# Kernel tuning notes

Measured on AMD Instinct MI355X. Metric: run time of the kernel, lower is better.

The kernel has to match this reference:

```python
import jax, jax.numpy as jnp
import numpy as np


def setup_inputs() -> dict:
    key = jax.random.key(0)
    kx, kq, kv = jax.random.split(key, 3)
    B, S, D = 4, 2048, 64
    # positive inputs + nonnegative W_Q guarantee diagonal scores > threshold t=1,
    # so no softmax column is fully -inf (the original would NaN on symmetric data).
    x = jax.random.uniform(kx, (B, S, D), dtype=jnp.float32)
    std = 1.0 / np.sqrt(S)  # xavier_normal for an SxS matrix: sqrt(2/(S+S))
    W_Q = jnp.abs(jax.random.normal(kq, (S, S), dtype=jnp.float32) * std)
    W_V = jax.random.normal(kv, (S, S), dtype=jnp.float32) * std
    return {"x": x, "W_Q": W_Q, "W_V": W_V}


def reference(x, W_Q, W_V):
    B, S, D = x.shape
    t = 1.0  # sigma threshold
    neg_inf = jnp.asarray(-jnp.inf, x.dtype)

    # V = W_V @ T  (contract over the token axis)
    V = jnp.einsum('st,btd->bsd', W_V, x)

    # G = running mean of tokens (cumsum / position). Original divides by
    # arange(0, S) which is a divide-by-zero bug at position 0; we use the
    # intended running-mean denominator 1..S.
    denom = jnp.arange(1, S + 1, dtype=x.dtype)[None, :, None]  # [1,S,1]
    G = jnp.cumsum(x, axis=1) / denom

    Q = jnp.einsum('st,btd->bsd', W_Q, G)          # [B,S,D]
    scores = jnp.einsum('bid,bjd->bij', Q, x)      # Q @ K^T, K = x

    # sigma: values <= t -> -inf
    scores = jnp.where(scores <= t, neg_inf, scores)

    # causal mask M: -inf strictly above the diagonal
    causal = jnp.triu(jnp.full((S, S), neg_inf, dtype=x.dtype), k=1)
    A = scores + causal

    # NOTE: original softmax is over dim=1 (the query axis), kept faithfully.
    P = jax.nn.softmax(A / jnp.sqrt(jnp.asarray(S, x.dtype)), axis=1)
    return jnp.einsum('bij,bjd->bid', P, V)
```

## Files before the change

kernel.cpp:

```cpp
#include <hip/hip_runtime.h>

typedef unsigned short u16;
typedef __bf16 bf16;
typedef bf16 bf16x8 __attribute__((ext_vector_type(8)));
typedef float f32x4 __attribute__((ext_vector_type(4)));

#define S 2048
#define D 64
#define BATCH 4
#define SCL 0.022097086912079612f

__device__ __forceinline__ u16 f2bf(float f) {
  union { float f; unsigned u; } v; v.f = f;
  return (u16)((v.u + 0x7FFFu + ((v.u >> 16) & 1u)) >> 16);
}

__device__ __forceinline__ void gld16(const u16* g, u16* l) {
  __builtin_amdgcn_global_load_lds(
      (const __attribute__((address_space(1))) unsigned int*)(const void*)g,
      (__attribute__((address_space(3))) unsigned int*)(void*)l, 16, 0, 0);
}

__global__ void k_pre(const float* __restrict__ x,
                      const float* __restrict__ wq, const float* __restrict__ wv,
                      u16* __restrict__ wqp, u16* __restrict__ wvb,
                      u16* __restrict__ xb, u16* __restrict__ xTb,
                      float* __restrict__ out) {
  int bx = blockIdx.x, t = threadIdx.x;
  if (bx < 512) {
    int m = bx * 4 + (t >> 6);
    int l = t & 63;
    const float* row = wq + (size_t)m * S;
    u16* orow = wqp + (size_t)m * S;
    float carry = 0.f;
    for (int c = 31; c >= 0; --c) {
      int tt = c * 64 + l;
      float a = row[tt] / (float)(tt + 1);
      float s = a;
#pragma unroll
      for (int off = 1; off < 64; off <<= 1) {
        float o = __shfl_down(s, off);
        s += (l + off < 64) ? o : 0.f;
      }
      float tot = __shfl(s, 0);
      orow[tt] = f2bf(s + carry);
      carry += tot;
    }
  } else if (bx < 2560) {
    size_t idx = ((size_t)(bx - 512) * 256 + t) * 8;
    const float* src = wv + idx;
    float4 a = *(const float4*)src;
    float4 b = *(const float4*)(src + 4);
    union { u16 s[8]; uint4 v; } u;
    u.s[0]=f2bf(a.x); u.s[1]=f2bf(a.y); u.s[2]=f2bf(a.z); u.s[3]=f2bf(a.w);
    u.s[4]=f2bf(b.x); u.s[5]=f2bf(b.y); u.s[6]=f2bf(b.z); u.s[7]=f2bf(b.w);
    *(uint4*)(wvb + idx) = u.v;
  } else if (bx < 2688) {
    int job = (bx - 2560) * 4 + (t >> 6);
    int chunk = job >> 2, b = job & 3, d = t & 63;
    const float* xp = x + ((size_t)b * S + (size_t)chunk * 16) * D + d;
#pragma unroll
    for (int s = 0; s < 16; ++s) {
      float v = xp[(size_t)s * D];
      int sg = chunk * 16 + s;
      u16 h = f2bf(v);
      xb[((size_t)b * S + sg) * D + d] = h;
      xTb[((size_t)b * D + d) * S + sg] = h;
    }
  } else {
    size_t i = (((size_t)(bx - 2688) * 256) + t) * 4;
    *(float4*)(out + i) = make_float4(0.f, 0.f, 0.f, 0.f);
  }
}

__global__ __launch_bounds__(128) void k_wg(
    const u16* __restrict__ wqp, const u16* __restrict__ wvb,
    const u16* __restrict__ xTb,
    u16* __restrict__ Qb, u16* __restrict__ VTb) {
  __shared__ u16 Ab[2][64 * 64];
  __shared__ u16 Bb[2][32 * 64];
  int bx = blockIdx.x;
  int nt = bx >> 6, mm = bx & 63, mt = mm >> 1, mat = mm & 1;
  int t = threadIdx.x;
  int w = t >> 6, l = t & 63;
  int lr = l & 15, lg = l >> 4;
  const u16* A = (mat ? wvb : wqp) + (size_t)(mt * 64) * S;
  const u16* BT = xTb + (size_t)(nt * 32) * S;
  int rA = t >> 3;
  int sb = t & 7;
  int swz = (sb ^ (rA & 7)) * 8;
  const u16* Ag = A + (size_t)rA * S + swz;
  const u16* Bg = BT + (size_t)rA * S + swz;
  f32x4 acc[2][2] = {};

  auto stage = [&](int buf, int kt) {
#pragma unroll
    for (int i = 0; i < 4; ++i)
      gld16(Ag + kt * 64 + (size_t)i * 16 * S, &Ab[buf][i * 1024 + t * 8]);
#pragma unroll
    for (int i = 0; i < 2; ++i)
      gld16(Bg + kt * 64 + (size_t)i * 16 * S, &Bb[buf][i * 1024 + t * 8]);
  };

  stage(0, 0);
  __syncthreads();
  int buf = 0;
  for (int kt = 0; kt < 32; ++kt) {
    if (kt < 31) stage(buf ^ 1, kt + 1);
    bf16x8 af[2][2], bfv[2][2];
#pragma unroll
    for (int mf = 0; mf < 2; ++mf)
#pragma unroll
      for (int ks = 0; ks < 2; ++ks) {
        int row = w * 32 + mf * 16 + lr;
        af[mf][ks] = *(const bf16x8*)&Ab[buf][row * 64 + (((ks * 4 + lg) ^ (lr & 7)) * 8)];
      }
#pragma unroll
    for (int nf = 0; nf < 2; ++nf)
#pragma unroll
      for (int ks = 0; ks < 2; ++ks) {
        int row = nf * 16 + lr;
        bfv[nf][ks] = *(const bf16x8*)&Bb[buf][row * 64 + (((ks * 4 + lg) ^ (lr & 7)) * 8)];
      }
#pragma unroll
    for (int ks = 0; ks < 2; ++ks)
#pragma unroll
      for (int mf = 0; mf < 2; ++mf)
#pragma unroll
        for (int nf = 0; nf < 2; ++nf)
          acc[mf][nf] = __builtin_amdgcn_mfma_f32_16x16x32_bf16(af[mf][ks], bfv[nf][ks], acc[mf][nf], 0, 0, 0);
    __syncthreads();
    buf ^= 1;
  }
#pragma unroll
  for (int mf = 0; mf < 2; ++mf) {
    int mbase = mt * 64 + w * 32 + mf * 16 + lg * 4;
#pragma unroll
    for (int nf = 0; nf < 2; ++nf) {
      int n = nt * 32 + nf * 16 + lr;
      int b = n >> 6, d = n & 63;
      if (mat == 0) {
#pragma unroll
        for (int r = 0; r < 4; ++r)
          Qb[((size_t)b * S + mbase + r) * D + d] = f2bf(acc[mf][nf][r]);
      } else {
        union { u16 s[4]; ushort4 v; } u;
#pragma unroll
        for (int r = 0; r < 4; ++r) u.s[r] = f2bf(acc[mf][nf][r]);
        *(ushort4*)&VTb[((size_t)b * D + d) * S + mbase] = u.v;
      }
    }
  }
}

__global__ __launch_bounds__(256) void k_stats(
    const u16* __restrict__ xb, const u16* __restrict__ Qb,
    float* __restrict__ rzbuf) {
  __shared__ float zs[4][16];
  int jg = blockIdx.x, b = blockIdx.y;
  int tid = threadIdx.x;
  int w = tid >> 6, l = tid & 63;
  int lr = l & 15, lg = l >> 4;
  int j0 = jg * 16;
  const u16* xbase = xb + (size_t)b * S * D;
  const u16* qbase = Qb + (size_t)b * S * D;
  bf16x8 xa0 = *(const bf16x8*)(xbase + (size_t)(j0 + lr) * D + lg * 8);
  bf16x8 xa1 = *(const bf16x8*)(xbase + (size_t)(j0 + lr) * D + 32 + lg * 8);
  float z[4] = {0.f, 0.f, 0.f, 0.f};
  for (int i16 = j0 + w * 16; i16 < S; i16 += 64) {
    bf16x8 q0 = *(const bf16x8*)(qbase + (size_t)(i16 + lr) * D + lg * 8);
    bf16x8 q1 = *(const bf16x8*)(qbase + (size_t)(i16 + lr) * D + 32 + lg * 8);
    f32x4 c = {};
    c = __builtin_amdgcn_mfma_f32_16x16x32_bf16(xa0, q0, c, 0, 0, 0);
    c = __builtin_amdgcn_mfma_f32_16x16x32_bf16(xa1, q1, c, 0, 0, 0);
    int i = i16 + lr;
#pragma unroll
    for (int r = 0; r < 4; ++r) {
      int j = j0 + lg * 4 + r;
      float sc = c[r];
      z[r] += (i >= j && sc > 1.0f) ? __expf(sc * SCL) : 0.f;
    }
  }
#pragma unroll
  for (int r = 0; r < 4; ++r) {
    z[r] += __shfl_xor(z[r], 1);
    z[r] += __shfl_xor(z[r], 2);
    z[r] += __shfl_xor(z[r], 4);
    z[r] += __shfl_xor(z[r], 8);
  }
  if (lr == 0) {
#pragma unroll
    for (int r = 0; r < 4; ++r) zs[w][lg * 4 + r] = z[r];
  }
  __syncthreads();
  if (tid < 16) {
    float zf = zs[0][tid] + zs[1][tid] + zs[2][tid] + zs[3][tid];
    rzbuf[(size_t)b * S + j0 + tid] = 1.0f / zf;
  }
}

__global__ __launch_bounds__(256) void k_out(
    const u16* __restrict__ xb, const u16* __restrict__ Qb, const u16* __restrict__ VTb,
    const float* __restrict__ rzbuf, float* __restrict__ out) {
  __shared__ u16 Plds[4][16][72];
  int bx = 143 - blockIdx.x, b = blockIdx.y;
  int it = 0, jc = 0, base = 0;
  for (int tt = 0; tt < 32; ++tt) {
    int nc = (tt + 4) >> 2;
    if (bx < base + nc) { it = tt; jc = bx - base; break; }
    base += nc;
  }
  int w = threadIdx.x >> 6, l = threadIdx.x & 63;
  int lr = l & 15, lg = l >> 4;
  int i0 = it * 64 + w * 16;
  const u16* xbase = xb + (size_t)b * S * D;
  const u16* qbase = Qb + (size_t)b * S * D;
  const u16* vbase = VTb + (size_t)b * D * S;
  const float* rzb = rzbuf + (size_t)b * S;
  bf16x8 qa0 = *(const bf16x8*)(qbase + (size_t)(i0 + lr) * D + lg * 8);
  bf16x8 qa1 = *(const bf16x8*)(qbase + (size_t)(i0 + lr) * D + 32 + lg * 8);
  f32x4 acc[4] = {};
  int jt_end = min(jc * 4 + 4, it + 1);
  for (int jt = jc * 4; jt < jt_end; ++jt) {
#pragma unroll
    for (int js = 0; js < 4; ++js) {
      int j16 = jt * 64 + js * 16;
      bf16x8 xb0 = *(const bf16x8*)(xbase + (size_t)(j16 + lr) * D + lg * 8);
      bf16x8 xb1 = *(const bf16x8*)(xbase + (size_t)(j16 + lr) * D + 32 + lg * 8);
      f32x4 c = {};
      c = __builtin_amdgcn_mfma_f32_16x16x32_bf16(qa0, xb0, c, 0, 0, 0);
      c = __builtin_amdgcn_mfma_f32_16x16x32_bf16(qa1, xb1, c, 0, 0, 0);
      int j = j16 + lr;
      float rzj = rzb[j];
#pragma unroll
      for (int r = 0; r < 4; ++r) {
        int i = i0 + lg * 4 + r;
        float sc = c[r];
        float wgt = (j <= i && sc > 1.0f) ? __expf(sc * SCL) * rzj : 0.f;
        Plds[w][lg * 4 + r][js * 16 + lr] = f2bf(wgt);
      }
    }
    asm volatile("s_waitcnt lgkmcnt(0)" ::: "memory");
#pragma unroll
    for (int kk = 0; kk < 2; ++kk) {
      bf16x8 pa = *(const bf16x8*)(&Plds[w][lr][kk * 32 + lg * 8]);
#pragma unroll
      for (int dt = 0; dt < 4; ++dt) {
        bf16x8 vbf = *(const bf16x8*)(vbase + (size_t)(dt * 16 + lr) * S + jt * 64 + kk * 32 + lg * 8);
        acc[dt] = __builtin_amdgcn_mfma_f32_16x16x32_bf16(pa, vbf, acc[dt], 0, 0, 0);
      }
    }
    asm volatile("s_waitcnt lgkmcnt(0)" ::: "memory");
  }
  float* obase = out + (size_t)b * S * D;
#pragma unroll
  for (int dt = 0; dt < 4; ++dt)
#pragma unroll
    for (int r = 0; r < 4; ++r) {
      int i = i0 + lg * 4 + r;
      atomicAdd(&obase[(size_t)i * D + dt * 16 + lr], acc[dt][r]);
    }
}

extern "C" void kernel_launch(void* const* d_in, const int* in_sizes, int n_in,
                              void* d_out, int out_size, void* d_ws, size_t ws_size,
                              hipStream_t stream) {
  const float* x  = (const float*)d_in[0];
  const float* wq = (const float*)d_in[1];
  const float* wv = (const float*)d_in[2];
  float* out = (float*)d_out;
  char* ws = (char*)d_ws;
  size_t off = 0;
  auto alloc = [&](size_t bytes) -> void* {
    void* p = ws + off; off += (bytes + 255) & ~255ULL; return p;
  };
  u16* xb   = (u16*)alloc((size_t)BATCH * S * D * 2);
  u16* xTb  = (u16*)alloc((size_t)BATCH * S * D * 2);
  u16* Qb   = (u16*)alloc((size_t)BATCH * S * D * 2);
  u16* VTb  = (u16*)alloc((size_t)BATCH * S * D * 2);
  float* rzbuf = (float*)alloc((size_t)BATCH * S * 4);
  u16* wqp  = (u16*)alloc((size_t)S * S * 2);
  u16* wvb  = (u16*)alloc((size_t)S * S * 2);

  k_pre<<<3200, 256, 0, stream>>>(x, wq, wv, wqp, wvb, xb, xTb, out);
  k_wg<<<512, 128, 0, stream>>>(wqp, wvb, xTb, Qb, VTb);
  k_stats<<<dim3(128, BATCH), 256, 0, stream>>>(xb, Qb, rzbuf);
  k_out<<<dim3(144, BATCH), 256, 0, stream>>>(xb, Qb, VTb, rzbuf, out);
}
```

Baseline: 81.90 us.

## Fuse stats and output kernels with per-tile counters; vectorize W_Q suffix scan

Merges the column-normalizer kernel and the output kernel into one launch. Stats blocks publish 1/Z per 64-column tile by bumping an atomic counter. Output blocks compute their QK^T tiles first, then spin-wait on that counter before applying the normalizer, which removes a launch boundary and lets the two phases overlap. The W_Q prefix-scan preprocessing is also changed to load float4 per lane and run 8 wave scans instead of 32. The spin-wait risks stalls or deadlock if output blocks occupy the GPU before the stats blocks are scheduled; the fixed block ordering is meant to mitigate this.

```diff
diff --git a/kernel.cpp b/kernel.cpp
--- a/kernel.cpp
+++ b/kernel.cpp
@@ -25,25 +25,42 @@
                       const float* __restrict__ wq, const float* __restrict__ wv,
                       u16* __restrict__ wqp, u16* __restrict__ wvb,
                       u16* __restrict__ xb, u16* __restrict__ xTb,
-                      float* __restrict__ out) {
+                      float* __restrict__ out, int* __restrict__ cnt) {
   int bx = blockIdx.x, t = threadIdx.x;
   if (bx < 512) {
     int m = bx * 4 + (t >> 6);
     int l = t & 63;
     const float* row = wq + (size_t)m * S;
     u16* orow = wqp + (size_t)m * S;
+    float4 f[8];
+#pragma unroll
+    for (int c = 0; c < 8; ++c) f[c] = *(const float4*)(row + c * 256 + l * 4);
+#pragma unroll
+    for (int c = 0; c < 8; ++c) {
+      int base = c * 256 + l * 4;
+      f[c].x /= (float)(base + 1); f[c].y /= (float)(base + 2);
+      f[c].z /= (float)(base + 3); f[c].w /= (float)(base + 4);
+    }
     float carry = 0.f;
-    for (int c = 31; c >= 0; --c) {
-      int tt = c * 64 + l;
-      float a = row[tt] / (float)(tt + 1);
-      float s = a;
+#pragma unroll
+    for (int c = 7; c >= 0; --c) {
+      float4 v = f[c];
+      float sl = v.x + v.y + v.z + v.w;
+      float s = sl;
 #pragma unroll
       for (int off = 1; off < 64; off <<= 1) {
         float o = __shfl_down(s, off);
         s += (l + off < 64) ? o : 0.f;
       }
       float tot = __shfl(s, 0);
-      orow[tt] = f2bf(s + carry);
+      float excl = s - sl;
+      float s3 = v.w, s2 = v.z + s3, s1 = v.y + s2, s0 = v.x + s1;
+      union { u16 q[4]; ushort4 u4; } o;
+      o.q[0] = f2bf(carry + excl + s0);
+      o.q[1] = f2bf(carry + excl + s1);
+      o.q[2] = f2bf(carry + excl + s2);
+      o.q[3] = f2bf(carry + excl + s3);
+      *(ushort4*)(orow + c * 256 + l * 4) = o.u4;
       carry += tot;
     }
   } else if (bx < 2560) {
@@ -68,6 +85,7 @@
       xTb[((size_t)b * D + d) * S + sg] = h;
     }
   } else {
+    if (bx == 2688 && t < 128) cnt[t] = 0;
     size_t i = (((size_t)(bx - 2688) * 256) + t) * 4;
     *(float4*)(out + i) = make_float4(0.f, 0.f, 0.f, 0.f);
   }
@@ -153,113 +171,125 @@
   }
 }
 
-__global__ __launch_bounds__(256) void k_stats(
-    const u16* __restrict__ xb, const u16* __restrict__ Qb,
-    float* __restrict__ rzbuf) {
+__global__ __launch_bounds__(256) void k_su(
+    const u16* __restrict__ xb, const u16* __restrict__ Qb, const u16* __restrict__ VTb,
+    float* __restrict__ rzbuf, int* __restrict__ cnt, float* __restrict__ out) {
+  __shared__ u16 Plds[4][16][72];
   __shared__ float zs[4][16];
-  int jg = blockIdx.x, b = blockIdx.y;
+  int bx = blockIdx.x, b = blockIdx.y;
   int tid = threadIdx.x;
   int w = tid >> 6, l = tid & 63;
   int lr = l & 15, lg = l >> 4;
-  int j0 = jg * 16;
   const u16* xbase = xb + (size_t)b * S * D;
   const u16* qbase = Qb + (size_t)b * S * D;
-  bf16x8 xa0 = *(const bf16x8*)(xbase + (size_t)(j0 + lr) * D + lg * 8);
-  bf16x8 xa1 = *(const bf16x8*)(xbase + (size_t)(j0 + lr) * D + 32 + lg * 8);
-  float z[4] = {0.f, 0.f, 0.f, 0.f};
-  for (int i16 = j0 + w * 16; i16 < S; i16 += 64) {
-    bf16x8 q0 = *(const bf16x8*)(qbase + (size_t)(i16 + lr) * D + lg * 8);
-    bf16x8 q1 = *(const bf16x8*)(qbase + (size_t)(i16 + lr) * D + 32 + lg * 8);
-    f32x4 c = {};
-    c = __builtin_amdgcn_mfma_f32_16x16x32_bf16(xa0, q0, c, 0, 0, 0);
-    c = __builtin_amdgcn_mfma_f32_16x16x32_bf16(xa1, q1, c, 0, 0, 0);
-    int i = i16 + lr;
+
+  if (bx < 128) {
+    int jg = bx;
+    int j0 = jg * 16;
+    bf16x8 xa0 = *(const bf16x8*)(xbase + (size_t)(j0 + lr) * D + lg * 8);
+    bf16x8 xa1 = *(const bf16x8*)(xbase + (size_t)(j0 + lr) * D + 32 + lg * 8);
+    float z[4] = {0.f, 0.f, 0.f, 0.f};
+    for (int i16 = j0 + w * 16; i16 < S; i16 += 64) {
+      bf16x8 q0 = *(const bf16x8*)(qbase + (size_t)(i16 + lr) * D + lg * 8);
+      bf16x8 q1 = *(const bf16x8*)(qbase + (size_t)(i16 + lr) * D + 32 + lg * 8);
+      f32x4 c = {};
+      c = __builtin_amdgcn_mfma_f32_16x16x32_bf16(xa0, q0, c, 0, 0, 0);
+      c = __builtin_amdgcn_mfma_f32_16x16x32_bf16(xa1, q1, c, 0, 0, 0);
+      int i = i16 + lr;
+#pragma unroll
+      for (int r = 0; r < 4; ++r) {
+        int j = j0 + lg * 4 + r;
+        float sc = c[r];
+        z[r] += (i >= j && sc > 1.0f) ? __expf(sc * SCL) : 0.f;
+      }
+    }
 #pragma unroll
     for (int r = 0; r < 4; ++r) {
-      int j = j0 + lg * 4 + r;
-      float sc = c[r];
-      z[r] += (i >= j && sc > 1.0f) ? __expf(sc * SCL) : 0.f;
-    }
-  }
-#pragma unroll
-  for (int r = 0; r < 4; ++r) {
-    z[r] += __shfl_xor(z[r], 1);
-    z[r] += __shfl_xor(z[r], 2);
-    z[r] += __shfl_xor(z[r], 4);
-    z[r] += __shfl_xor(z[r], 8);
-  }
-  if (lr == 0) {
-#pragma unroll
-    for (int r = 0; r < 4; ++r) zs[w][lg * 4 + r] = z[r];
-  }
-  __syncthreads();
-  if (tid < 16) {
-    float zf = zs[0][tid] + zs[1][tid] + zs[2][tid] + zs[3][tid];
-    rzbuf[(size_t)b * S + j0 + tid] = 1.0f / zf;
-  }
-}
-
-__global__ __launch_bounds__(256) void k_out(
-    const u16* __restrict__ xb, const u16* __restrict__ Qb, const u16* __restrict__ VTb,
-    const float* __restrict__ rzbuf, float* __restrict__ out) {
-  __shared__ u16 Plds[4][16][72];
-  int bx = 143 - blockIdx.x, b = blockIdx.y;
-  int it = 0, jc = 0, base = 0;
-  for (int tt = 0; tt < 32; ++tt) {
-    int nc = (tt + 4) >> 2;
-    if (bx < base + nc) { it = tt; jc = bx - base; break; }
-    base += nc;
-  }
-  int w = threadIdx.x >> 6, l = threadIdx.x & 63;
-  int lr = l & 15, lg = l >> 4;
-  int i0 = it * 64 + w * 16;
-  const u16* xbase = xb + (size_t)b * S * D;
-  const u16* qbase = Qb + (size_t)b * S * D;
-  const u16* vbase = VTb + (size_t)b * D * S;
-  const float* rzb = rzbuf + (size_t)b * S;
-  bf16x8 qa0 = *(const bf16x8*)(qbase + (size_t)(i0 + lr) * D + lg * 8);
-  bf16x8 qa1 = *(const bf16x8*)(qbase + (size_t)(i0 + lr) * D + 32 + lg * 8);
-  f32x4 acc[4] = {};
-  int jt_end = min(jc * 4 + 4, it + 1);
-  for (int jt = jc * 4; jt < jt_end; ++jt) {
-#pragma unroll
-    for (int js = 0; js < 4; ++js) {
-      int j16 = jt * 64 + js * 16;
-      bf16x8 xb0 = *(const bf16x8*)(xbase + (size_t)(j16 + lr) * D + lg * 8);
-      bf16x8 xb1 = *(const bf16x8*)(xbase + (size_t)(j16 + lr) * D + 32 + lg * 8);
-      f32x4 c = {};
-      c = __builtin_amdgcn_mfma_f32_16x16x32_bf16(qa0, xb0, c, 0, 0, 0);
-      c = __builtin_amdgcn_mfma_f32_16x16x32_bf16(qa1, xb1, c, 0, 0, 0);
-      int j = j16 + lr;
-      float rzj = rzb[j];
+      z[r] += __shfl_xor(z[r], 1);
+      z[r] += __shfl_xor(z[r], 2);
+      z[r] += __shfl_xor(z[r], 4);
+      z[r] += __shfl_xor(z[r], 8);
+    }
+    if (lr == 0) {
+#pragma unroll
+      for (int r = 0; r < 4; ++r) zs[w][lg * 4 + r] = z[r];
+    }
+    __syncthreads();
+    if (tid < 16) {
+      float zf = zs[0][tid] + zs[1][tid] + zs[2][tid] + zs[3][tid];
+      rzbuf[(size_t)b * S + j0 + tid] = 1.0f / zf;
+    }
+    __threadfence();
+    if (tid == 0)
+      __hip_atomic_fetch_add(&cnt[b * 32 + (jg >> 2)], 1,
+                             __ATOMIC_RELEASE, __HIP_MEMORY_SCOPE_AGENT);
+  } else {
+    int obx = 143 - (bx - 128);
+    int it = 0, jc = 0, base = 0;
+    for (int tt = 0; tt < 32; ++tt) {
+      int nc = (tt + 4) >> 2;
+      if (obx < base + nc) { it = tt; jc = obx - base; break; }
+      base += nc;
+    }
+    int i0 = it * 64 + w * 16;
+    const u16* vbase = VTb + (size_t)b * D * S;
+    const float* rzb = rzbuf + (size_t)b * S;
+    bf16x8 qa0 = *(const bf16x8*)(qbase + (size_t)(i0 + lr) * D + lg * 8);
+    bf16x8 qa1 = *(const bf16x8*)(qbase + (size_t)(i0 + lr) * D + 32 + lg * 8);
+    f32x4 acc[4] = {};
+    int jt_end = min(jc * 4 + 4, it + 1);
+    for (int jt = jc * 4; jt < jt_end; ++jt) {
+      f32x4 c4[4];
+#pragma unroll
+      for (int js = 0; js < 4; ++js) {
+        int j16 = jt * 64 + js * 16;
+        bf16x8 xb0 = *(const bf16x8*)(xbase + (size_t)(j16 + lr) * D + lg * 8);
+        bf16x8 xb1 = *(const bf16x8*)(xbase + (size_t)(j16 + lr) * D + 32 + lg * 8);
+        f32x4 c = {};
+        c = __builtin_amdgcn_mfma_f32_16x16x32_bf16(qa0, xb0, c, 0, 0, 0);
+        c = __builtin_amdgcn_mfma_f32_16x16x32_bf16(qa1, xb1, c, 0, 0, 0);
+        c4[js] = c;
+      }
+      if (tid == 0) {
+        while (__hip_atomic_load(&cnt[b * 32 + jt], __ATOMIC_RELAXED,
+                                 __HIP_MEMORY_SCOPE_AGENT) < 4)
+          __builtin_amdgcn_s_sleep(2);
+      }
+      __syncthreads();
+      __threadfence();
+#pragma unroll
+      for (int js = 0; js < 4; ++js) {
+        int j = jt * 64 + js * 16 + lr;
+        float rzj = rzb[j];
+#pragma unroll
+        for (int r = 0; r < 4; ++r) {
+          int i = i0 + lg * 4 + r;
+          float sc = c4[js][r];
+          float wgt = (j <= i && sc > 1.0f) ? __expf(sc * SCL) * rzj : 0.f;
+          Plds[w][lg * 4 + r][js * 16 + lr] = f2bf(wgt);
+        }
+      }
+      asm volatile("s_waitcnt lgkmcnt(0)" ::: "memory");
+#pragma unroll
+      for (int kk = 0; kk < 2; ++kk) {
+        bf16x8 pa = *(const bf16x8*)(&Plds[w][lr][kk * 32 + lg * 8]);
+#pragma unroll
+        for (int dt = 0; dt < 4; ++dt) {
+          bf16x8 vbf = *(const bf16x8*)(vbase + (size_t)(dt * 16 + lr) * S + jt * 64 + kk * 32 + lg * 8);
+          acc[dt] = __builtin_amdgcn_mfma_f32_16x16x32_bf16(pa, vbf, acc[dt], 0, 0, 0);
+        }
+      }
+      asm volatile("s_waitcnt lgkmcnt(0)" ::: "memory");
+    }
+    float* obase = out + (size_t)b * S * D;
+#pragma unroll
+    for (int dt = 0; dt < 4; ++dt)
 #pragma unroll
       for (int r = 0; r < 4; ++r) {
         int i = i0 + lg * 4 + r;
-        float sc = c[r];
-        float wgt = (j <= i && sc > 1.0f) ? __expf(sc * SCL) * rzj : 0.f;
-        Plds[w][lg * 4 + r][js * 16 + lr] = f2bf(wgt);
-      }
-    }
-    asm volatile("s_waitcnt lgkmcnt(0)" ::: "memory");
-#pragma unroll
-    for (int kk = 0; kk < 2; ++kk) {
-      bf16x8 pa = *(const bf16x8*)(&Plds[w][lr][kk * 32 + lg * 8]);
-#pragma unroll
-      for (int dt = 0; dt < 4; ++dt) {
-        bf16x8 vbf = *(const bf16x8*)(vbase + (size_t)(dt * 16 + lr) * S + jt * 64 + kk * 32 + lg * 8);
-        acc[dt] = __builtin_amdgcn_mfma_f32_16x16x32_bf16(pa, vbf, acc[dt], 0, 0, 0);
-      }
-    }
-    asm volatile("s_waitcnt lgkmcnt(0)" ::: "memory");
+        atomicAdd(&obase[(size_t)i * D + dt * 16 + lr], acc[dt][r]);
+      }
   }
-  float* obase = out + (size_t)b * S * D;
-#pragma unroll
-  for (int dt = 0; dt < 4; ++dt)
-#pragma unroll
-    for (int r = 0; r < 4; ++r) {
-      int i = i0 + lg * 4 + r;
-      atomicAdd(&obase[(size_t)i * D + dt * 16 + lr], acc[dt][r]);
-    }
 }
 
 extern "C" void kernel_launch(void* const* d_in, const int* in_sizes, int n_in,
@@ -279,11 +309,11 @@
   u16* Qb   = (u16*)alloc((size_t)BATCH * S * D * 2);
   u16* VTb  = (u16*)alloc((size_t)BATCH * S * D * 2);
   float* rzbuf = (float*)alloc((size_t)BATCH * S * 4);
+  int*   cnt   = (int*)alloc((size_t)BATCH * 32 * 4);
   u16* wqp  = (u16*)alloc((size_t)S * S * 2);
   u16* wvb  = (u16*)alloc((size_t)S * S * 2);
 
-  k_pre<<<3200, 256, 0, stream>>>(x, wq, wv, wqp, wvb, xb, xTb, out);
+  k_pre<<<3200, 256, 0, stream>>>(x, wq, wv, wqp, wvb, xb, xTb, out, cnt);
   k_wg<<<512, 128, 0, stream>>>(wqp, wvb, xTb, Qb, VTb);
-  k_stats<<<dim3(128, BATCH), 256, 0, stream>>>(xb, Qb, rzbuf);
-  k_out<<<dim3(144, BATCH), 256, 0, stream>>>(xb, Qb, VTb, rzbuf, out);
-}
+  k_su<<<dim3(272, BATCH), 256, 0, stream>>>(xb, Qb, VTb, rzbuf, cnt, out);
+}
```

Measured after the change: 264.7 us. 223% more time.
